# Performance work log

Hardware: AMD Instinct MI355X
Metric: run time of the kernel (lower is better)

The kernel has to match this reference:

```python
import jax, jax.numpy as jnp
import numpy as np

N_NODES = 500000


def gcn_conv(x, edge_index, W, b, n_nodes):
    # PyG GCNConv: h = x @ W; add self-loops; symmetric deg normalization;
    # scatter-add messages to target nodes; add bias.
    h = x @ W                                # [N, out]
    row, col = edge_index[0], edge_index[1]  # source -> target
    ones = jnp.ones(row.shape, dtype=h.dtype)
    deg = jax.ops.segment_sum(ones, col, num_segments=n_nodes) + 1.0  # +1 self-loop
    dinv = jnp.where(deg > 0, deg ** -0.5, 0.0)
    norm = dinv[row] * dinv[col]             # [E]
    msg = h[row] * norm[:, None]             # [E, out]
    agg = jax.ops.segment_sum(msg, col, num_segments=n_nodes)
    agg = agg + (dinv * dinv)[:, None] * h   # self-loop contribution
    return agg + b


def setup_inputs() -> dict:
    key = jax.random.key(0)
    k1, k2, k3, k4, k5, k6 = jax.random.split(key, 6)
    x = jax.random.normal(k1, (N_NODES, 9), dtype=jnp.float32)
    edge_index = jax.random.randint(k2, (2, 16000000), 0, N_NODES, dtype=jnp.int64)
    # Glorot-style init for GCN weights, zero bias (PyG default bias=True)
    W1 = jax.random.uniform(k3, (9, 4), jnp.float32, -1.0, 1.0) * (6.0 / (9 + 4)) ** 0.5
    b1 = jnp.zeros((4,), jnp.float32)
    W2 = jax.random.uniform(k4, (4, 2), jnp.float32, -1.0, 1.0) * (6.0 / (4 + 2)) ** 0.5
    b2 = jnp.zeros((2,), jnp.float32)
    return {"x": x, "edge_index": edge_index, "W1": W1, "b1": b1, "W2": W2, "b2": b2}


def reference(x, edge_index, W1, b1, W2, b2):
    h = gcn_conv(x, edge_index, W1, b1, N_NODES)
    h = jnp.tanh(h)
    h = gcn_conv(h, edge_index, W2, b2, N_NODES)
    return h
```

## Files before the change

### kernel.cpp

```cpp
#include <hip/hip_runtime.h>
#include <hip/hip_fp16.h>
#include <math.h>

#define NN 500000
#define BSZ 512
#define NBK ((NN + BSZ - 1) / BSZ)
#define SCH 8192
#define KMAX 20

typedef __attribute__((ext_vector_type(4))) _Float16 half4;
typedef __attribute__((ext_vector_type(2))) _Float16 half2v;
typedef __attribute__((ext_vector_type(4))) int int4v;

__global__ void hist_kernel(const int* __restrict__ col, unsigned short* __restrict__ blkCnt,
                            int E, int nch) {
    __shared__ int cnt[4 * 1024];
    int t = threadIdx.x;
    for (int i = t; i < 4096; i += 256) cnt[i] = 0;
    __syncthreads();
    int base = blockIdx.x * (4 * SCH);
    int end = base + 4 * SCH; if (end > E) end = E;
    for (int j = base + t * 4; j < end; j += 1024) {
        int4v c = __builtin_nontemporal_load(reinterpret_cast<const int4v*>(col + j));
        int sub = (j - base) >> 13;
        atomicAdd(&cnt[sub * 1024 + (c.x >> 9)], 1);
        atomicAdd(&cnt[sub * 1024 + (c.y >> 9)], 1);
        atomicAdd(&cnt[sub * 1024 + (c.z >> 9)], 1);
        atomicAdd(&cnt[sub * 1024 + (c.w >> 9)], 1);
    }
    __syncthreads();
    int chunk0 = blockIdx.x * 4;
#pragma unroll
    for (int s = 0; s < 4; ++s) {
        int c = chunk0 + s;
        if (c >= nch) break;
        for (int b = t; b < 1024; b += 256)
            blkCnt[(size_t)c * 1024 + b] = (unsigned short)cnt[s * 1024 + b];
    }
}

__global__ void colscan_kernel(unsigned short* __restrict__ blkCnt,
                               int* __restrict__ bucketTotal, int nch) {
    __shared__ int ls[64][5];
    int t = threadIdx.x;
    int cl = t & 3;
    int bk = t >> 2;
    int b = blockIdx.x * 4 + cl;
    int cps = (nch + 63) >> 6;
    int c0 = bk * cps;
    int c1 = c0 + cps; if (c1 > nch) c1 = nch;
    int run = 0;
    for (int c = c0; c < c1; ++c)
        run += blkCnt[(size_t)c * 1024 + b];
    ls[bk][cl] = run;
    __syncthreads();
    if (t < 4) {
        int r = 0;
        for (int k = 0; k < 64; ++k) { int v = ls[k][t]; ls[k][t] = r; r += v; }
        bucketTotal[blockIdx.x * 4 + t] = r;
    }
    __syncthreads();
    int running = ls[bk][cl];
    for (int c = c0; c < c1; ++c) {
        size_t idx = (size_t)c * 1024 + b;
        int v = blkCnt[idx];
        blkCnt[idx] = (unsigned short)running;
        running += v;
    }
}

__global__ void scan_kernel(const int* __restrict__ bucketTotal, int* __restrict__ bucketStart) {
    __shared__ int ls[1024];
    int t = threadIdx.x;
    int v = bucketTotal[t];
    ls[t] = v;
    __syncthreads();
    for (int off = 1; off < 1024; off <<= 1) {
        int u = (t >= off) ? ls[t - off] : 0;
        __syncthreads();
        ls[t] += u;
        __syncthreads();
    }
    bucketStart[t] = ls[t] - v;
}

__global__ __launch_bounds__(256) void part_kernel(const int* __restrict__ row,
                                                   const int* __restrict__ col,
                                                   const int* __restrict__ bucketStart,
                                                   const int* __restrict__ bucketTotal,
                                                   const unsigned short* __restrict__ blkPre,
                                                   int* __restrict__ recs, int E, int nch) {
    __shared__ int gbase[1024];
    __shared__ int lexcl[1024];
    __shared__ int cursor[1024];
    __shared__ int ts[256];
    __shared__ int srt[SCH];
    __shared__ unsigned short bkt[SCH];
    int t = threadIdx.x;
    int chunk = blockIdx.x;
    const unsigned short* pre = blkPre + (size_t)chunk * 1024;
    const unsigned short* nxt = blkPre + (size_t)(chunk + 1) * 1024;
    bool last = (chunk == nch - 1);
    int myc[4];
#pragma unroll
    for (int k = 0; k < 4; ++k) {
        int b = t * 4 + k;
        int p = pre[b];
        int n = last ? bucketTotal[b] : (int)nxt[b];
        myc[k] = n - p;
        gbase[b] = bucketStart[b] + p;
    }
    int tsum = myc[0] + myc[1] + myc[2] + myc[3];
    ts[t] = tsum;
    __syncthreads();
    for (int off = 1; off < 256; off <<= 1) {
        int u = (t >= off) ? ts[t - off] : 0;
        __syncthreads();
        ts[t] += u;
        __syncthreads();
    }
    int r = ts[t] - tsum;
#pragma unroll
    for (int k = 0; k < 4; ++k) {
        int b = t * 4 + k;
        lexcl[b] = r;
        cursor[b] = r;
        r += myc[k];
    }
    __syncthreads();
    int base = chunk * SCH;
    int end = base + SCH; if (end > E) end = E;
    for (int j = base + t * 4; j < end; j += 1024) {
        int4v rr = __builtin_nontemporal_load(reinterpret_cast<const int4v*>(row + j));
        int4v cc = __builtin_nontemporal_load(reinterpret_cast<const int4v*>(col + j));
        int b, rk;
        b = cc.x >> 9; rk = atomicAdd(&cursor[b], 1); srt[rk] = (rr.x << 9) | (cc.x & 511); bkt[rk] = (unsigned short)b;
        b = cc.y >> 9; rk = atomicAdd(&cursor[b], 1); srt[rk] = (rr.y << 9) | (cc.y & 511); bkt[rk] = (unsigned short)b;
        b = cc.z >> 9; rk = atomicAdd(&cursor[b], 1); srt[rk] = (rr.z << 9) | (cc.z & 511); bkt[rk] = (unsigned short)b;
        b = cc.w >> 9; rk = atomicAdd(&cursor[b], 1); srt[rk] = (rr.w << 9) | (cc.w & 511); bkt[rk] = (unsigned short)b;
    }
    __syncthreads();
    int m = end - base;
    for (int p = t; p < m; p += 256) {
        int b = bkt[p];
        recs[gbase[b] + (p - lexcl[b])] = srt[p];
    }
}

__global__ __launch_bounds__(1024) void sort_kernel(const int* __restrict__ bucketStart,
                                                    const int* __restrict__ bucketTotal,
                                                    int* __restrict__ recs,
                                                    float* __restrict__ dinv,
                                                    int* __restrict__ nodeStart, int N, int E) {
    __shared__ int cnt[BSZ];
    __shared__ int sc[BSZ];
    int t = threadIdx.x, b = blockIdx.x;
    int s = bucketStart[b], m = bucketTotal[b];
    int v[KMAX];
#pragma unroll
    for (int k = 0; k < KMAX; ++k) {
        int idx = t + k * 1024;
        v[k] = (idx < m) ? recs[s + idx] : -1;
    }
    if (t < BSZ) cnt[t] = 0;
    __syncthreads();
#pragma unroll
    for (int k = 0; k < KMAX; ++k)
        if (v[k] >= 0) atomicAdd(&cnt[v[k] & 511], 1);
    __syncthreads();
    if (t < BSZ) sc[t] = cnt[t];
    __syncthreads();
    for (int off = 1; off < BSZ; off <<= 1) {
        int u = 0;
        if (t < BSZ && t >= off) u = sc[t - off];
        __syncthreads();
        if (t < BSZ) sc[t] += u;
        __syncthreads();
    }
    if (t < BSZ) {
        int excl = sc[t] - cnt[t];
        int node = b * BSZ + t;
        if (node < N) {
            nodeStart[node] = s + excl;
            dinv[node] = rsqrtf((float)cnt[t] + 1.0f);
        }
        cnt[t] = excl;
    }
    if (b == NBK - 1 && t == 0) nodeStart[N] = E;
    __syncthreads();
#pragma unroll
    for (int k = 0; k < KMAX; ++k) {
        if (v[k] >= 0) {
            int rk = atomicAdd(&cnt[v[k] & 511], 1);
            recs[s + rk] = v[k] >> 9;
        }
    }
}

__global__ void prep_kernel(const float* __restrict__ x, const float* __restrict__ W1,
                            const float* __restrict__ dinv, half4* __restrict__ g1h, int N) {
    int i = blockIdx.x * blockDim.x + threadIdx.x;
    if (i >= N) return;
    float d = dinv[i];
    float acc0 = 0.f, acc1 = 0.f, acc2 = 0.f, acc3 = 0.f;
#pragma unroll
    for (int k = 0; k < 9; ++k) {
        float xv = x[i * 9 + k];
        acc0 += xv * W1[k * 4 + 0];
        acc1 += xv * W1[k * 4 + 1];
        acc2 += xv * W1[k * 4 + 2];
        acc3 += xv * W1[k * 4 + 3];
    }
    half4 h;
    h.x = (_Float16)(d * acc0);
    h.y = (_Float16)(d * acc1);
    h.z = (_Float16)(d * acc2);
    h.w = (_Float16)(d * acc3);
    g1h[i] = h;
}

__global__ void agg1_kernel(const int* __restrict__ nodeStart, const int* __restrict__ srows,
                            const float* __restrict__ dinv, const half4* __restrict__ g1h,
                            const float* __restrict__ b1, const float* __restrict__ W2,
                            half2v* __restrict__ g2h, int N) {
    int i = blockIdx.x * blockDim.x + threadIdx.x;
    if (i >= N) return;
    int s = nodeStart[i], e = nodeStart[i + 1];
    float a0 = 0.f, a1 = 0.f, a2 = 0.f, a3 = 0.f;
    int j = s;
    for (; j + 3 < e; j += 4) {
        int r0 = srows[j], r1 = srows[j + 1], r2 = srows[j + 2], r3 = srows[j + 3];
        half4 g0 = g1h[r0];
        half4 g1 = g1h[r1];
        half4 g2 = g1h[r2];
        half4 g3 = g1h[r3];
        a0 += (float)g0.x + (float)g1.x + (float)g2.x + (float)g3.x;
        a1 += (float)g0.y + (float)g1.y + (float)g2.y + (float)g3.y;
        a2 += (float)g0.z + (float)g1.z + (float)g2.z + (float)g3.z;
        a3 += (float)g0.w + (float)g1.w + (float)g2.w + (float)g3.w;
    }
    for (; j < e; ++j) {
        half4 g = g1h[srows[j]];
        a0 += (float)g.x; a1 += (float)g.y; a2 += (float)g.z; a3 += (float)g.w;
    }
    half4 self = g1h[i];
    float di = dinv[i];
    float t0 = tanhf(di * (a0 + (float)self.x) + b1[0]);
    float t1 = tanhf(di * (a1 + (float)self.y) + b1[1]);
    float t2 = tanhf(di * (a2 + (float)self.z) + b1[2]);
    float t3 = tanhf(di * (a3 + (float)self.w) + b1[3]);
    float o0 = t0 * W2[0] + t1 * W2[2] + t2 * W2[4] + t3 * W2[6];
    float o1 = t0 * W2[1] + t1 * W2[3] + t2 * W2[5] + t3 * W2[7];
    half2v g2o;
    g2o.x = (_Float16)(di * o0);
    g2o.y = (_Float16)(di * o1);
    g2h[i] = g2o;
}

__global__ void agg2_kernel(const int* __restrict__ nodeStart, const int* __restrict__ srows,
                            const float* __restrict__ dinv, const half2v* __restrict__ g2h,
                            const float* __restrict__ b2, float* __restrict__ out, int N) {
    int i = blockIdx.x * blockDim.x + threadIdx.x;
    if (i >= N) return;
    int s = nodeStart[i], e = nodeStart[i + 1];
    float a0 = 0.f, a1 = 0.f;
    int j = s;
    for (; j + 3 < e; j += 4) {
        int r0 = srows[j], r1 = srows[j + 1], r2 = srows[j + 2], r3 = srows[j + 3];
        half2v g0 = g2h[r0];
        half2v g1 = g2h[r1];
        half2v g2 = g2h[r2];
        half2v g3 = g2h[r3];
        a0 += (float)g0.x + (float)g1.x + (float)g2.x + (float)g3.x;
        a1 += (float)g0.y + (float)g1.y + (float)g2.y + (float)g3.y;
    }
    for (; j < e; ++j) {
        half2v g = g2h[srows[j]];
        a0 += (float)g.x; a1 += (float)g.y;
    }
    half2v self = g2h[i];
    float di = dinv[i];
    reinterpret_cast<float2*>(out)[i] =
        make_float2(di * (a0 + (float)self.x) + b2[0],
                    di * (a1 + (float)self.y) + b2[1]);
}

extern "C" void kernel_launch(void* const* d_in, const int* in_sizes, int n_in,
                              void* d_out, int out_size, void* d_ws, size_t ws_size,
                              hipStream_t stream) {
    const float* x  = (const float*)d_in[0];
    const int*   ei = (const int*)d_in[1];
    const float* W1 = (const float*)d_in[2];
    const float* b1 = (const float*)d_in[3];
    const float* W2 = (const float*)d_in[4];
    const float* b2 = (const float*)d_in[5];
    float* out = (float*)d_out;

    const int N = NN;
    const int E = in_sizes[1] / 2;
    const int* row = ei;
    const int* col = ei + E;

    const int nch = (E + SCH - 1) / SCH;

    char* ws = (char*)d_ws;
    size_t off = 0;
    int* bucketTotal = (int*)(ws + off);            off += 4096;
    int* bucketStart = (int*)(ws + off);            off += 4096;
    off = 16384;
    unsigned short* blkCnt = (unsigned short*)(ws + off);
    off += (size_t)(nch + 1) * 1024 * 2;
    off = (off + 15) & ~(size_t)15;
    float*  dinv      = (float*)(ws + off);         off += (size_t)NN * 4;
    off = (off + 15) & ~(size_t)15;
    half4*  g1h       = (half4*)(ws + off);         off += (size_t)NN * 8;
    off = (off + 15) & ~(size_t)15;
    half2v* g2h       = (half2v*)(ws + off);        off += (size_t)NN * 4;
    off = (off + 15) & ~(size_t)15;
    int*    nodeStart = (int*)(ws + off);           off += (size_t)(NN + 1) * 4;
    off = (off + 15) & ~(size_t)15;
    int*    recs      = (int*)(ws + off);

    (void)hipMemsetAsync(blkCnt + (size_t)nch * 1024, 0, 2048, stream);

    const int ngrid = (N + 255) / 256;
    const int hgrid = (nch + 3) / 4;

    hist_kernel   <<<hgrid, 256, 0, stream>>>(col, blkCnt, E, nch);
    colscan_kernel<<<256, 256, 0, stream>>>(blkCnt, bucketTotal, nch);
    scan_kernel   <<<1, 1024, 0, stream>>>(bucketTotal, bucketStart);
    part_kernel   <<<nch, 256, 0, stream>>>(row, col, bucketStart, bucketTotal, blkCnt, recs, E, nch);
    sort_kernel   <<<NBK, 1024, 0, stream>>>(bucketStart, bucketTotal, recs, dinv, nodeStart, N, E);
    prep_kernel   <<<ngrid, 256, 0, stream>>>(x, W1, dinv, g1h, N);
    agg1_kernel   <<<ngrid, 256, 0, stream>>>(nodeStart, recs, dinv, g1h, b1, W2, g2h, N);
    agg2_kernel   <<<ngrid, 256, 0, stream>>>(nodeStart, recs, dinv, g2h, b2, out, N);
}
```

Before: 709.7 us.

## Replace per-node sort with bucket-level shared-memory atomic aggregation

Drops the second-level counting sort that produced per-node CSR segments. Degree counting and both aggregation passes now run per 512-node bucket, scattering gathered features into shared-memory float accumulators with atomics. The prep kernel also stages x through shared memory for coalesced loads. This removes a full read/write pass over the edge records and the nodeStart array, at the cost of many LDS atomics per edge and non-deterministic float summation order.

After: 819.0 us. +15.4%, slower.

```diff
diff --git a/kernel.cpp b/kernel.cpp
--- a/kernel.cpp
+++ b/kernel.cpp
@@ -6,11 +6,11 @@
 #define BSZ 512
 #define NBK ((NN + BSZ - 1) / BSZ)
 #define SCH 8192
-#define KMAX 20
 
 typedef __attribute__((ext_vector_type(4))) _Float16 half4;
 typedef __attribute__((ext_vector_type(2))) _Float16 half2v;
 typedef __attribute__((ext_vector_type(4))) int int4v;
+typedef __attribute__((ext_vector_type(2))) float float2v;
 
 __global__ void hist_kernel(const int* __restrict__ col, unsigned short* __restrict__ blkCnt,
                             int E, int nch) {
@@ -147,65 +147,51 @@
     }
 }
 
-__global__ __launch_bounds__(1024) void sort_kernel(const int* __restrict__ bucketStart,
-                                                    const int* __restrict__ bucketTotal,
-                                                    int* __restrict__ recs,
-                                                    float* __restrict__ dinv,
-                                                    int* __restrict__ nodeStart, int N, int E) {
+__global__ __launch_bounds__(256) void deg_kernel(const int* __restrict__ bucketStart,
+                                                  const int* __restrict__ bucketTotal,
+                                                  const int* __restrict__ recs,
+                                                  float* __restrict__ dinv, int N) {
     __shared__ int cnt[BSZ];
-    __shared__ int sc[BSZ];
     int t = threadIdx.x, b = blockIdx.x;
-    int s = bucketStart[b], m = bucketTotal[b];
-    int v[KMAX];
-#pragma unroll
-    for (int k = 0; k < KMAX; ++k) {
-        int idx = t + k * 1024;
-        v[k] = (idx < m) ? recs[s + idx] : -1;
-    }
-    if (t < BSZ) cnt[t] = 0;
-    __syncthreads();
-#pragma unroll
-    for (int k = 0; k < KMAX; ++k)
-        if (v[k] >= 0) atomicAdd(&cnt[v[k] & 511], 1);
-    __syncthreads();
-    if (t < BSZ) sc[t] = cnt[t];
-    __syncthreads();
-    for (int off = 1; off < BSZ; off <<= 1) {
-        int u = 0;
-        if (t < BSZ && t >= off) u = sc[t - off];
-        __syncthreads();
-        if (t < BSZ) sc[t] += u;
-        __syncthreads();
-    }
-    if (t < BSZ) {
-        int excl = sc[t] - cnt[t];
-        int node = b * BSZ + t;
-        if (node < N) {
-            nodeStart[node] = s + excl;
-            dinv[node] = rsqrtf((float)cnt[t] + 1.0f);
-        }
-        cnt[t] = excl;
-    }
-    if (b == NBK - 1 && t == 0) nodeStart[N] = E;
-    __syncthreads();
-#pragma unroll
-    for (int k = 0; k < KMAX; ++k) {
-        if (v[k] >= 0) {
-            int rk = atomicAdd(&cnt[v[k] & 511], 1);
-            recs[s + rk] = v[k] >> 9;
-        }
-    }
-}
-
-__global__ void prep_kernel(const float* __restrict__ x, const float* __restrict__ W1,
-                            const float* __restrict__ dinv, half4* __restrict__ g1h, int N) {
-    int i = blockIdx.x * blockDim.x + threadIdx.x;
+    cnt[t] = 0; cnt[t + 256] = 0;
+    __syncthreads();
+    int s = bucketStart[b], e = s + bucketTotal[b];
+    int sA = (s + 3) & ~3; if (sA > e) sA = e;
+    int eA = sA + ((e - sA) & ~3);
+    if (t < sA - s) atomicAdd(&cnt[recs[s + t] & 511], 1);
+    if (t >= 4 && t - 4 < e - eA) atomicAdd(&cnt[recs[eA + (t - 4)] & 511], 1);
+    for (int j = sA + 4 * t; j + 3 < e; j += 1024) {
+        int4v q = __builtin_nontemporal_load(reinterpret_cast<const int4v*>(recs + j));
+        atomicAdd(&cnt[q.x & 511], 1);
+        atomicAdd(&cnt[q.y & 511], 1);
+        atomicAdd(&cnt[q.z & 511], 1);
+        atomicAdd(&cnt[q.w & 511], 1);
+    }
+    __syncthreads();
+    int n0 = b * BSZ + t;
+    if (n0 < N) dinv[n0] = rsqrtf((float)cnt[t] + 1.0f);
+    int n1 = n0 + 256;
+    if (n1 < N) dinv[n1] = rsqrtf((float)cnt[t + 256] + 1.0f);
+}
+
+__global__ __launch_bounds__(256) void prep_kernel(const float* __restrict__ x,
+                                                   const float* __restrict__ W1,
+                                                   const float* __restrict__ dinv,
+                                                   half4* __restrict__ g1h, int N) {
+    __shared__ float xs[256 * 9];
+    int t = threadIdx.x;
+    int base = blockIdx.x * 256;
+    int nval = (N - base < 256 ? N - base : 256) * 9;
+    const float* xb = x + (size_t)base * 9;
+    for (int k = t; k < nval; k += 256) xs[k] = xb[k];
+    __syncthreads();
+    int i = base + t;
     if (i >= N) return;
     float d = dinv[i];
     float acc0 = 0.f, acc1 = 0.f, acc2 = 0.f, acc3 = 0.f;
 #pragma unroll
     for (int k = 0; k < 9; ++k) {
-        float xv = x[i * 9 + k];
+        float xv = xs[t * 9 + k];
         acc0 += xv * W1[k * 4 + 0];
         acc1 += xv * W1[k * 4 + 1];
         acc2 += xv * W1[k * 4 + 2];
@@ -219,70 +205,121 @@
     g1h[i] = h;
 }
 
-__global__ void agg1_kernel(const int* __restrict__ nodeStart, const int* __restrict__ srows,
-                            const float* __restrict__ dinv, const half4* __restrict__ g1h,
-                            const float* __restrict__ b1, const float* __restrict__ W2,
-                            half2v* __restrict__ g2h, int N) {
-    int i = blockIdx.x * blockDim.x + threadIdx.x;
-    if (i >= N) return;
-    int s = nodeStart[i], e = nodeStart[i + 1];
-    float a0 = 0.f, a1 = 0.f, a2 = 0.f, a3 = 0.f;
-    int j = s;
-    for (; j + 3 < e; j += 4) {
-        int r0 = srows[j], r1 = srows[j + 1], r2 = srows[j + 2], r3 = srows[j + 3];
-        half4 g0 = g1h[r0];
-        half4 g1 = g1h[r1];
-        half4 g2 = g1h[r2];
-        half4 g3 = g1h[r3];
-        a0 += (float)g0.x + (float)g1.x + (float)g2.x + (float)g3.x;
-        a1 += (float)g0.y + (float)g1.y + (float)g2.y + (float)g3.y;
-        a2 += (float)g0.z + (float)g1.z + (float)g2.z + (float)g3.z;
-        a3 += (float)g0.w + (float)g1.w + (float)g2.w + (float)g3.w;
-    }
-    for (; j < e; ++j) {
-        half4 g = g1h[srows[j]];
-        a0 += (float)g.x; a1 += (float)g.y; a2 += (float)g.z; a3 += (float)g.w;
-    }
-    half4 self = g1h[i];
-    float di = dinv[i];
-    float t0 = tanhf(di * (a0 + (float)self.x) + b1[0]);
-    float t1 = tanhf(di * (a1 + (float)self.y) + b1[1]);
-    float t2 = tanhf(di * (a2 + (float)self.z) + b1[2]);
-    float t3 = tanhf(di * (a3 + (float)self.w) + b1[3]);
-    float o0 = t0 * W2[0] + t1 * W2[2] + t2 * W2[4] + t3 * W2[6];
-    float o1 = t0 * W2[1] + t1 * W2[3] + t2 * W2[5] + t3 * W2[7];
-    half2v g2o;
-    g2o.x = (_Float16)(di * o0);
-    g2o.y = (_Float16)(di * o1);
-    g2h[i] = g2o;
-}
-
-__global__ void agg2_kernel(const int* __restrict__ nodeStart, const int* __restrict__ srows,
-                            const float* __restrict__ dinv, const half2v* __restrict__ g2h,
-                            const float* __restrict__ b2, float* __restrict__ out, int N) {
-    int i = blockIdx.x * blockDim.x + threadIdx.x;
-    if (i >= N) return;
-    int s = nodeStart[i], e = nodeStart[i + 1];
-    float a0 = 0.f, a1 = 0.f;
-    int j = s;
-    for (; j + 3 < e; j += 4) {
-        int r0 = srows[j], r1 = srows[j + 1], r2 = srows[j + 2], r3 = srows[j + 3];
-        half2v g0 = g2h[r0];
-        half2v g1 = g2h[r1];
-        half2v g2 = g2h[r2];
-        half2v g3 = g2h[r3];
-        a0 += (float)g0.x + (float)g1.x + (float)g2.x + (float)g3.x;
-        a1 += (float)g0.y + (float)g1.y + (float)g2.y + (float)g3.y;
-    }
-    for (; j < e; ++j) {
-        half2v g = g2h[srows[j]];
-        a0 += (float)g.x; a1 += (float)g.y;
-    }
-    half2v self = g2h[i];
-    float di = dinv[i];
-    reinterpret_cast<float2*>(out)[i] =
-        make_float2(di * (a0 + (float)self.x) + b2[0],
-                    di * (a1 + (float)self.y) + b2[1]);
+__global__ __launch_bounds__(256) void agg1_kernel(const int* __restrict__ bucketStart,
+                                                   const int* __restrict__ bucketTotal,
+                                                   const int* __restrict__ recs,
+                                                   const float* __restrict__ dinv,
+                                                   const half4* __restrict__ g1h,
+                                                   const float* __restrict__ b1,
+                                                   const float* __restrict__ W2,
+                                                   half2v* __restrict__ g2h, int N) {
+    __shared__ float acc[4][BSZ];
+    int t = threadIdx.x, b = blockIdx.x;
+#pragma unroll
+    for (int k = 0; k < 4; ++k) { acc[k][t] = 0.f; acc[k][t + 256] = 0.f; }
+    __syncthreads();
+    int s = bucketStart[b], e = s + bucketTotal[b];
+    int sA = (s + 3) & ~3; if (sA > e) sA = e;
+    int eA = sA + ((e - sA) & ~3);
+    if (t < sA - s) {
+        int v = recs[s + t]; half4 g = g1h[v >> 9]; int n = v & 511;
+        atomicAdd(&acc[0][n], (float)g.x); atomicAdd(&acc[1][n], (float)g.y);
+        atomicAdd(&acc[2][n], (float)g.z); atomicAdd(&acc[3][n], (float)g.w);
+    }
+    if (t >= 4 && t - 4 < e - eA) {
+        int v = recs[eA + (t - 4)]; half4 g = g1h[v >> 9]; int n = v & 511;
+        atomicAdd(&acc[0][n], (float)g.x); atomicAdd(&acc[1][n], (float)g.y);
+        atomicAdd(&acc[2][n], (float)g.z); atomicAdd(&acc[3][n], (float)g.w);
+    }
+#pragma unroll 2
+    for (int j = sA + 4 * t; j + 3 < e; j += 1024) {
+        int4v q = __builtin_nontemporal_load(reinterpret_cast<const int4v*>(recs + j));
+        half4 g0 = g1h[q.x >> 9];
+        half4 g1 = g1h[q.y >> 9];
+        half4 g2 = g1h[q.z >> 9];
+        half4 g3 = g1h[q.w >> 9];
+        int n0 = q.x & 511, n1 = q.y & 511, n2 = q.z & 511, n3 = q.w & 511;
+        atomicAdd(&acc[0][n0], (float)g0.x); atomicAdd(&acc[1][n0], (float)g0.y);
+        atomicAdd(&acc[2][n0], (float)g0.z); atomicAdd(&acc[3][n0], (float)g0.w);
+        atomicAdd(&acc[0][n1], (float)g1.x); atomicAdd(&acc[1][n1], (float)g1.y);
+        atomicAdd(&acc[2][n1], (float)g1.z); atomicAdd(&acc[3][n1], (float)g1.w);
+        atomicAdd(&acc[0][n2], (float)g2.x); atomicAdd(&acc[1][n2], (float)g2.y);
+        atomicAdd(&acc[2][n2], (float)g2.z); atomicAdd(&acc[3][n2], (float)g2.w);
+        atomicAdd(&acc[0][n3], (float)g3.x); atomicAdd(&acc[1][n3], (float)g3.y);
+        atomicAdd(&acc[2][n3], (float)g3.z); atomicAdd(&acc[3][n3], (float)g3.w);
+    }
+    __syncthreads();
+#pragma unroll
+    for (int h = 0; h < 2; ++h) {
+        int n = t + h * 256;
+        int node = b * BSZ + n;
+        if (node < N) {
+            half4 self = g1h[node];
+            float di = dinv[node];
+            float t0 = tanhf(di * (acc[0][n] + (float)self.x) + b1[0]);
+            float t1 = tanhf(di * (acc[1][n] + (float)self.y) + b1[1]);
+            float t2 = tanhf(di * (acc[2][n] + (float)self.z) + b1[2]);
+            float t3 = tanhf(di * (acc[3][n] + (float)self.w) + b1[3]);
+            float o0 = t0 * W2[0] + t1 * W2[2] + t2 * W2[4] + t3 * W2[6];
+            float o1 = t0 * W2[1] + t1 * W2[3] + t2 * W2[5] + t3 * W2[7];
+            half2v g2o;
+            g2o.x = (_Float16)(di * o0);
+            g2o.y = (_Float16)(di * o1);
+            g2h[node] = g2o;
+        }
+    }
+}
+
+__global__ __launch_bounds__(256) void agg2_kernel(const int* __restrict__ bucketStart,
+                                                   const int* __restrict__ bucketTotal,
+                                                   const int* __restrict__ recs,
+                                                   const float* __restrict__ dinv,
+                                                   const half2v* __restrict__ g2h,
+                                                   const float* __restrict__ b2,
+                                                   float* __restrict__ out, int N) {
+    __shared__ float acc[2][BSZ];
+    int t = threadIdx.x, b = blockIdx.x;
+#pragma unroll
+    for (int k = 0; k < 2; ++k) { acc[k][t] = 0.f; acc[k][t + 256] = 0.f; }
+    __syncthreads();
+    int s = bucketStart[b], e = s + bucketTotal[b];
+    int sA = (s + 3) & ~3; if (sA > e) sA = e;
+    int eA = sA + ((e - sA) & ~3);
+    if (t < sA - s) {
+        int v = recs[s + t]; half2v g = g2h[v >> 9]; int n = v & 511;
+        atomicAdd(&acc[0][n], (float)g.x); atomicAdd(&acc[1][n], (float)g.y);
+    }
+    if (t >= 4 && t - 4 < e - eA) {
+        int v = recs[eA + (t - 4)]; half2v g = g2h[v >> 9]; int n = v & 511;
+        atomicAdd(&acc[0][n], (float)g.x); atomicAdd(&acc[1][n], (float)g.y);
+    }
+#pragma unroll 2
+    for (int j = sA + 4 * t; j + 3 < e; j += 1024) {
+        int4v q = __builtin_nontemporal_load(reinterpret_cast<const int4v*>(recs + j));
+        half2v g0 = g2h[q.x >> 9];
+        half2v g1 = g2h[q.y >> 9];
+        half2v g2 = g2h[q.z >> 9];
+        half2v g3 = g2h[q.w >> 9];
+        int n0 = q.x & 511, n1 = q.y & 511, n2 = q.z & 511, n3 = q.w & 511;
+        atomicAdd(&acc[0][n0], (float)g0.x); atomicAdd(&acc[1][n0], (float)g0.y);
+        atomicAdd(&acc[0][n1], (float)g1.x); atomicAdd(&acc[1][n1], (float)g1.y);
+        atomicAdd(&acc[0][n2], (float)g2.x); atomicAdd(&acc[1][n2], (float)g2.y);
+        atomicAdd(&acc[0][n3], (float)g3.x); atomicAdd(&acc[1][n3], (float)g3.y);
+    }
+    __syncthreads();
+#pragma unroll
+    for (int h = 0; h < 2; ++h) {
+        int n = t + h * 256;
+        int node = b * BSZ + n;
+        if (node < N) {
+            half2v self = g2h[node];
+            float di = dinv[node];
+            float2v o;
+            o.x = di * (acc[0][n] + (float)self.x) + b2[0];
+            o.y = di * (acc[1][n] + (float)self.y) + b2[1];
+            __builtin_nontemporal_store(o, reinterpret_cast<float2v*>(out) + node);
+        }
+    }
 }
 
 extern "C" void kernel_launch(void* const* d_in, const int* in_sizes, int n_in,
@@ -317,8 +354,6 @@
     off = (off + 15) & ~(size_t)15;
     half2v* g2h       = (half2v*)(ws + off);        off += (size_t)NN * 4;
     off = (off + 15) & ~(size_t)15;
-    int*    nodeStart = (int*)(ws + off);           off += (size_t)(NN + 1) * 4;
-    off = (off + 15) & ~(size_t)15;
     int*    recs      = (int*)(ws + off);
 
     (void)hipMemsetAsync(blkCnt + (size_t)nch * 1024, 0, 2048, stream);
@@ -330,8 +365,8 @@
     colscan_kernel<<<256, 256, 0, stream>>>(blkCnt, bucketTotal, nch);
     scan_kernel   <<<1, 1024, 0, stream>>>(bucketTotal, bucketStart);
     part_kernel   <<<nch, 256, 0, stream>>>(row, col, bucketStart, bucketTotal, blkCnt, recs, E, nch);
-    sort_kernel   <<<NBK, 1024, 0, stream>>>(bucketStart, bucketTotal, recs, dinv, nodeStart, N, E);
+    deg_kernel    <<<NBK, 256, 0, stream>>>(bucketStart, bucketTotal, recs, dinv, N);
     prep_kernel   <<<ngrid, 256, 0, stream>>>(x, W1, dinv, g1h, N);
-    agg1_kernel   <<<ngrid, 256, 0, stream>>>(nodeStart, recs, dinv, g1h, b1, W2, g2h, N);
-    agg2_kernel   <<<ngrid, 256, 0, stream>>>(nodeStart, recs, dinv, g2h, b2, out, N);
-}
+    agg1_kernel   <<<NBK, 256, 0, stream>>>(bucketStart, bucketTotal, recs, dinv, g1h, b1, W2, g2h, N);
+    agg2_kernel   <<<NBK, 256, 0, stream>>>(bucketStart, bucketTotal, recs, dinv, g2h, b2, out, N);
+}
```
